# Kernel tuning notes

Measured on AMD Instinct MI355X. Metric: run time of the kernel, lower is better.

## Reference

```python
import jax, jax.numpy as jnp
import numpy as np

BATCH, SEQ, DIM = 32, 1024, 512

def setup_inputs() -> dict:
    key = jax.random.key(0)
    k1, k2, k3 = jax.random.split(key, 3)
    scale = 1.0 / np.sqrt(DIM)
    return {
        "embedded_sequence": jax.random.normal(k1, (BATCH, SEQ, DIM), dtype=jnp.float32),
        "W_xh": jax.random.normal(k2, (DIM, DIM), dtype=jnp.float32) * scale,
        "W_hh": jax.random.normal(k3, (DIM, DIM), dtype=jnp.float32) * scale,
        "b": jnp.zeros((DIM,), dtype=jnp.float32),
    }

def reference(embedded_sequence, W_xh, W_hh, b):
    # SimpleRNN: h_t = tanh(x_t @ W_xh + h_{t-1} @ W_hh + b)
    B, T, D = embedded_sequence.shape
    # Precompute input projection for all timesteps (one big GEMM)
    xw = jnp.einsum('btd,de->bte', embedded_sequence, W_xh) + b  # [B,T,D]
    h0 = jnp.zeros((B, D), dtype=embedded_sequence.dtype)

    def step(h, xw_t):
        h_new = jnp.tanh(xw_t + h @ W_hh)
        return h_new, h_new

    h_final, seq_out = jax.lax.scan(step, h0, jnp.swapaxes(xw, 0, 1))  # scan over T
    seq_out = jnp.swapaxes(seq_out, 0, 1)  # [B,T,D]
    return (seq_out, h_final)
```

## Files before the change

kernel.cpp:

```cpp
#include <hip/hip_runtime.h>
#include <hip/hip_fp16.h>

#define BATCH 32
#define SEQ   1024
#define DIM   512

typedef _Float16 f16x8 __attribute__((ext_vector_type(8)));
typedef float    f32x4 __attribute__((ext_vector_type(4)));
typedef unsigned int u32x4 __attribute__((ext_vector_type(4)));

union UU4 { uint4 s; u32x4 v; };

static __device__ __forceinline__ float tanh_fast(float x) {
    float e = __expf(2.0f * x);
    return 1.0f - 2.0f / (e + 1.0f);
}

__global__ void pack_w(const float* __restrict__ W, __half* __restrict__ Wp) {
    int id = blockIdx.x * blockDim.x + threadIdx.x;
    int n = id & 511;
    int k = id >> 9;
    Wp[((k >> 5) * 512 + n) * 32 + ((k >> 3) & 3) * 8 + (k & 7)] = __float2half(W[k * 512 + n]);
}

__global__ __launch_bounds__(256) void gemm_xw(const float* __restrict__ X,
                                               const __half* __restrict__ Wp,
                                               const float* __restrict__ bias,
                                               float* __restrict__ out) {
    const int nb   = blockIdx.x;
    const int mb   = blockIdx.y;
    const int lane = threadIdx.x & 63;
    const int wave = threadIdx.x >> 6;
    const int q    = lane >> 4;
    const int r16  = lane & 15;
    const int row  = mb * 64 + wave * 16 + r16;

    const float4* Xf4  = (const float4*)X;
    const uint4*  WpU4 = (const uint4*)Wp;

    f32x4 acc[4];
    #pragma unroll
    for (int nt = 0; nt < 4; ++nt) acc[nt] = (f32x4){0.f, 0.f, 0.f, 0.f};

    #pragma unroll 4
    for (int kb = 0; kb < 16; ++kb) {
        float4 a0 = Xf4[row * 128 + kb * 8 + q * 2];
        float4 a1 = Xf4[row * 128 + kb * 8 + q * 2 + 1];
        f16x8 af;
        af[0] = (_Float16)a0.x; af[1] = (_Float16)a0.y;
        af[2] = (_Float16)a0.z; af[3] = (_Float16)a0.w;
        af[4] = (_Float16)a1.x; af[5] = (_Float16)a1.y;
        af[6] = (_Float16)a1.z; af[7] = (_Float16)a1.w;
        #pragma unroll
        for (int nt = 0; nt < 4; ++nt) {
            int col = nb * 64 + nt * 16 + r16;
            UU4 tmp; tmp.s = WpU4[(kb * 512 + col) * 4 + q];
            acc[nt] = __builtin_amdgcn_mfma_f32_16x16x32_f16(
                af, __builtin_bit_cast(f16x8, tmp.v), acc[nt], 0, 0, 0);
        }
    }

    const int rbase = mb * 64 + wave * 16 + q * 4;
    #pragma unroll
    for (int nt = 0; nt < 4; ++nt) {
        int col = nb * 64 + nt * 16 + r16;
        float bv = bias[col];
        #pragma unroll
        for (int rr = 0; rr < 4; ++rr) {
            out[(size_t)(rbase + rr) * 512 + col] = acc[nt][rr] + bv;
        }
    }
}

__global__ __launch_bounds__(512, 2) void rnn_rec(const uint4* __restrict__ Wp4,
                                                  float* __restrict__ out) {
    extern __shared__ char smem[];
    uint4*  LBS = (uint4*)smem;
    __half* hb  = (__half*)(smem + 131072);

    const int b    = blockIdx.x;
    const int t    = threadIdx.x;
    const int lane = t & 63;
    const int w    = t >> 6;
    const int q    = lane >> 4;
    const int r16  = lane & 15;

    #pragma unroll
    for (int j = 0; j < 16; ++j) {
        int kb  = 12 + (j >> 2);
        int col = w * 64 + (j & 3) * 16 + r16;
        LBS[j * 512 + t] = Wp4[(kb * 512 + col) * 4 + q];
    }

    u32x4 Bf[48];
    #pragma unroll
    for (int kb = 0; kb < 12; ++kb) {
        #pragma unroll
        for (int nt = 0; nt < 4; ++nt) {
            int col = w * 64 + nt * 16 + r16;
            UU4 tmp; tmp.s = Wp4[(kb * 512 + col) * 4 + q];
            Bf[kb * 4 + nt] = tmp.v;
        }
    }
    #pragma unroll
    for (int i = 0; i < 48; ++i) asm volatile("" : "+a"(Bf[i]));

    float* orow = out + (size_t)b * SEQ * DIM;
    const int c = w * 64 + q * 16 + r16;

    float xw = orow[c];
    float h  = tanh_fast(xw);
    orow[c] = h;
    hb[c] = __float2half(h);
    xw = orow[DIM + c];
    __syncthreads();

    #pragma unroll 1
    for (int step = 1; step < SEQ; ++step) {
        orow += DIM;
        const __half* ha = hb + (((step & 1) ^ 1) << 9);

        f32x4 m[4];
        #pragma unroll
        for (int i = 0; i < 4; ++i) m[i] = (f32x4){0.f, 0.f, 0.f, 0.f};

        #pragma unroll
        for (int s = 0; s < 4; ++s) {
            f16x8 af = *(const f16x8*)(ha + (12 + s) * 32 + q * 8);
            #pragma unroll
            for (int nt = 0; nt < 4; ++nt) {
                UU4 tmp; tmp.s = LBS[(s * 4 + nt) * 512 + t];
                m[nt] = __builtin_amdgcn_mfma_f32_16x16x32_f16(
                    af, __builtin_bit_cast(f16x8, tmp.v), m[nt], 0, 0, 0);
            }
        }
        #pragma unroll
        for (int kb = 0; kb < 12; ++kb) {
            f16x8 af = *(const f16x8*)(ha + kb * 32 + q * 8);
            #pragma unroll
            for (int nt = 0; nt < 4; ++nt) {
                m[nt] = __builtin_amdgcn_mfma_f32_16x16x32_f16(
                    af, __builtin_bit_cast(f16x8, Bf[kb * 4 + nt]), m[nt], 0, 0, 0);
            }
        }

        float v = (q == 0 ? m[0][0] : q == 1 ? m[1][0] : q == 2 ? m[2][0] : m[3][0]) + xw;
        h = tanh_fast(v);

        orow[c] = h;
        __half* hw = hb + ((step & 1) << 9);
        hw[c] = __float2half(h);
        xw = orow[DIM + c];
        __syncthreads();
    }

    float* hf = out + (size_t)BATCH * SEQ * DIM + (size_t)b * DIM;
    hf[c] = h;
}

extern "C" void kernel_launch(void* const* d_in, const int* in_sizes, int n_in,
                              void* d_out, int out_size, void* d_ws, size_t ws_size,
                              hipStream_t stream) {
    const float* X    = (const float*)d_in[0];
    const float* Wxh  = (const float*)d_in[1];
    const float* Whh  = (const float*)d_in[2];
    const float* bias = (const float*)d_in[3];
    float* out = (float*)d_out;

    __half* WpXh = (__half*)d_ws;
    __half* WpHh = (__half*)((char*)d_ws + (512u << 10));

    (void)hipFuncSetAttribute((const void*)rnn_rec,
                              hipFuncAttributeMaxDynamicSharedMemorySize, 133120);

    pack_w<<<512, 512, 0, stream>>>(Wxh, WpXh);
    pack_w<<<512, 512, 0, stream>>>(Whh, WpHh);
    gemm_xw<<<dim3(8, 512), 256, 0, stream>>>(X, WpXh, bias, out);
    rnn_rec<<<BATCH, 512, 133120, stream>>>((const uint4*)WpHh, out);
}
```

Before: 1.509 ms.

## Stream part of W_hh from global each step, widen GEMM tiles, relax barrier

The recurrent kernel now keeps only the last two k-blocks of W_hh in LDS, halving shared memory. It re-reads two k-blocks from global/L2 into registers every step, with the loads issued between MFMA groups so their latency is hidden. The next-step xw load is hoisted to the start of the loop, and __syncthreads is replaced by a raw lgkmcnt wait plus s_barrier. Separately, the input-projection GEMM tile widens from 64 to 256 columns per block, raising reuse of X but also register pressure. The raw barrier does not wait on vmcnt, and the per-step global reads add L2 traffic to the serial critical path.

```diff
diff --git a/kernel.cpp b/kernel.cpp
--- a/kernel.cpp
+++ b/kernel.cpp
@@ -15,6 +15,8 @@
     float e = __expf(2.0f * x);
     return 1.0f - 2.0f / (e + 1.0f);
 }
+
+#define LDS_BARRIER() asm volatile("s_waitcnt lgkmcnt(0)\n\ts_barrier" ::: "memory")
 
 __global__ void pack_w(const float* __restrict__ W, __half* __restrict__ Wp) {
     int id = blockIdx.x * blockDim.x + threadIdx.x;
@@ -38,11 +40,11 @@
     const float4* Xf4  = (const float4*)X;
     const uint4*  WpU4 = (const uint4*)Wp;
 
-    f32x4 acc[4];
-    #pragma unroll
-    for (int nt = 0; nt < 4; ++nt) acc[nt] = (f32x4){0.f, 0.f, 0.f, 0.f};
-
-    #pragma unroll 4
+    f32x4 acc[16];
+    #pragma unroll
+    for (int nt = 0; nt < 16; ++nt) acc[nt] = (f32x4){0.f, 0.f, 0.f, 0.f};
+
+    #pragma unroll 2
     for (int kb = 0; kb < 16; ++kb) {
         float4 a0 = Xf4[row * 128 + kb * 8 + q * 2];
         float4 a1 = Xf4[row * 128 + kb * 8 + q * 2 + 1];
@@ -52,8 +54,8 @@
         af[4] = (_Float16)a1.x; af[5] = (_Float16)a1.y;
         af[6] = (_Float16)a1.z; af[7] = (_Float16)a1.w;
         #pragma unroll
-        for (int nt = 0; nt < 4; ++nt) {
-            int col = nb * 64 + nt * 16 + r16;
+        for (int nt = 0; nt < 16; ++nt) {
+            int col = nb * 256 + nt * 16 + r16;
             UU4 tmp; tmp.s = WpU4[(kb * 512 + col) * 4 + q];
             acc[nt] = __builtin_amdgcn_mfma_f32_16x16x32_f16(
                 af, __builtin_bit_cast(f16x8, tmp.v), acc[nt], 0, 0, 0);
@@ -62,8 +64,8 @@
 
     const int rbase = mb * 64 + wave * 16 + q * 4;
     #pragma unroll
-    for (int nt = 0; nt < 4; ++nt) {
-        int col = nb * 64 + nt * 16 + r16;
+    for (int nt = 0; nt < 16; ++nt) {
+        int col = nb * 256 + nt * 16 + r16;
         float bv = bias[col];
         #pragma unroll
         for (int rr = 0; rr < 4; ++rr) {
@@ -76,7 +78,7 @@
                                                   float* __restrict__ out) {
     extern __shared__ char smem[];
     uint4*  LBS = (uint4*)smem;
-    __half* hb  = (__half*)(smem + 131072);
+    __half* hb  = (__half*)(smem + 65536);
 
     const int b    = blockIdx.x;
     const int t    = threadIdx.x;
@@ -86,8 +88,8 @@
     const int r16  = lane & 15;
 
     #pragma unroll
-    for (int j = 0; j < 16; ++j) {
-        int kb  = 12 + (j >> 2);
+    for (int j = 0; j < 8; ++j) {
+        int kb  = 14 + (j >> 2);
         int col = w * 64 + (j & 3) * 16 + r16;
         LBS[j * 512 + t] = Wp4[(kb * 512 + col) * 4 + q];
     }
@@ -104,6 +106,17 @@
     }
     #pragma unroll
     for (int i = 0; i < 48; ++i) asm volatile("" : "+a"(Bf[i]));
+
+    const uint4* gp = Wp4 + ((size_t)(12 * 512 + w * 64 + r16)) * 4 + q;
+    u32x4 sbuf[8];
+    #pragma unroll
+    for (int s = 0; s < 2; ++s) {
+        #pragma unroll
+        for (int nt = 0; nt < 4; ++nt) {
+            UU4 tmp; tmp.s = gp[(s * 512 + nt * 16) * 4];
+            sbuf[s * 4 + nt] = tmp.v;
+        }
+    }
 
     float* orow = out + (size_t)b * SEQ * DIM;
     const int c = w * 64 + q * 16 + r16;
@@ -113,11 +126,13 @@
     orow[c] = h;
     hb[c] = __float2half(h);
     xw = orow[DIM + c];
-    __syncthreads();
+    LDS_BARRIER();
 
     #pragma unroll 1
     for (int step = 1; step < SEQ; ++step) {
         orow += DIM;
+        float xw_nxt = orow[DIM + c];
+
         const __half* ha = hb + (((step & 1) ^ 1) << 9);
 
         f32x4 m[4];
@@ -125,8 +140,8 @@
         for (int i = 0; i < 4; ++i) m[i] = (f32x4){0.f, 0.f, 0.f, 0.f};
 
         #pragma unroll
-        for (int s = 0; s < 4; ++s) {
-            f16x8 af = *(const f16x8*)(ha + (12 + s) * 32 + q * 8);
+        for (int s = 0; s < 2; ++s) {
+            f16x8 af = *(const f16x8*)(ha + (14 + s) * 32 + q * 8);
             #pragma unroll
             for (int nt = 0; nt < 4; ++nt) {
                 UU4 tmp; tmp.s = LBS[(s * 4 + nt) * 512 + t];
@@ -135,6 +150,23 @@
             }
         }
         #pragma unroll
+        for (int s = 0; s < 2; ++s) {
+            f16x8 af = *(const f16x8*)(ha + (12 + s) * 32 + q * 8);
+            #pragma unroll
+            for (int nt = 0; nt < 4; ++nt) {
+                m[nt] = __builtin_amdgcn_mfma_f32_16x16x32_f16(
+                    af, __builtin_bit_cast(f16x8, sbuf[s * 4 + nt]), m[nt], 0, 0, 0);
+            }
+        }
+        #pragma unroll
+        for (int s = 0; s < 2; ++s) {
+            #pragma unroll
+            for (int nt = 0; nt < 4; ++nt) {
+                UU4 tmp; tmp.s = gp[(s * 512 + nt * 16) * 4];
+                sbuf[s * 4 + nt] = tmp.v;
+            }
+        }
+        #pragma unroll
         for (int kb = 0; kb < 12; ++kb) {
             f16x8 af = *(const f16x8*)(ha + kb * 32 + q * 8);
             #pragma unroll
@@ -150,8 +182,8 @@
         orow[c] = h;
         __half* hw = hb + ((step & 1) << 9);
         hw[c] = __float2half(h);
-        xw = orow[DIM + c];
-        __syncthreads();
+        xw = xw_nxt;
+        LDS_BARRIER();
     }
 
     float* hf = out + (size_t)BATCH * SEQ * DIM + (size_t)b * DIM;
@@ -171,10 +203,10 @@
     __half* WpHh = (__half*)((char*)d_ws + (512u << 10));
 
     (void)hipFuncSetAttribute((const void*)rnn_rec,
-                              hipFuncAttributeMaxDynamicSharedMemorySize, 133120);
+                              hipFuncAttributeMaxDynamicSharedMemorySize, 67584);
 
     pack_w<<<512, 512, 0, stream>>>(Wxh, WpXh);
     pack_w<<<512, 512, 0, stream>>>(Whh, WpHh);
-    gemm_xw<<<dim3(8, 512), 256, 0, stream>>>(X, WpXh, bias, out);
-    rnn_rec<<<BATCH, 512, 133120, stream>>>((const uint4*)WpHh, out);
-}
+    gemm_xw<<<dim3(2, 512), 256, 0, stream>>>(X, WpXh, bias, out);
+    rnn_rec<<<BATCH, 512, 67584, stream>>>((const uint4*)WpHh, out);
+}
```

Result: slower. 2.392 ms (+58.5%).
